# Kernel optimization log

Measured on AMD Instinct MI355X. Metric: run time of the kernel, lower is better.

The kernel has to match this reference:

```python
import jax, jax.numpy as jnp
import numpy as np

E = 100000   # num entities
D = 300      # embedding dim
R = 1000     # num relations
T = 10000    # aligned pairs
K = 25       # negatives per pair
GAMMA = 1.0


def spmm(rows, cols, vals, x, n_rows):
    # sparse(COO) @ dense: out[r] = sum_{nnz: rows==r} vals * x[cols]
    return jax.ops.segment_sum(vals[:, None] * x[cols], rows, num_segments=n_rows)


def setup_inputs() -> dict:
    key = jax.random.key(0)
    ks = jax.random.split(key, 24)
    g = lambda i, s: jax.random.normal(ks[i], s, dtype=jnp.float32) * 0.05
    ri = lambda i, s, hi: jax.random.randint(ks[i], s, 0, hi, dtype=jnp.int32)
    ru = lambda i, s: jax.random.uniform(ks[i], s, dtype=jnp.float32)
    return {
        'word_embedding': jax.random.normal(ks[0], (E, D), dtype=jnp.float32),
        'kernel_gate': g(1, (D, D)),
        'bias_gate': jnp.zeros((D,), jnp.float32),
        'W1': g(2, (D, D)),
        'W2': g(3, (D, D)),
        'Dense': g(4, (3 * D, D)),
        'Bias': jnp.zeros((D,), jnp.float32),
        'hr_rows': ri(5, (300000,), R), 'hr_cols': ri(6, (300000,), E), 'hr_vals': ru(7, (300000,)),
        'tr_rows': ri(8, (300000,), R), 'tr_cols': ri(9, (300000,), E), 'tr_vals': ru(10, (300000,)),
        'er_rows': ri(11, (300000,), E), 'er_cols': ri(12, (300000,), 2 * R), 'er_vals': ru(13, (300000,)),
        'adj_rows': ri(14, (600000,), E), 'adj_cols': ri(15, (600000,), E), 'adj_vals': ru(16, (600000,)),
        'pos_left': ri(17, (T,), E), 'pos_right': ri(18, (T,), E),
        'neg_right': ri(19, (T, K), E), 'neg_left': ri(20, (T, K), E),
        'mask': jnp.ones((T, K), jnp.float32),
    }


def highway(layer1, layer2, kernel_gate, bias_gate):
    tg = jax.nn.sigmoid(layer1 @ kernel_gate + bias_gate)
    return tg * layer2 + (1.0 - tg) * layer1


def reference(word_embedding, kernel_gate, bias_gate, W1, W2, Dense, Bias,
              hr_rows, hr_cols, hr_vals, tr_rows, tr_cols, tr_vals,
              er_rows, er_cols, er_vals, adj_rows, adj_cols, adj_vals,
              pos_left, pos_right, neg_right, neg_left, mask):
    # L2-normalized frozen word embeddings
    emb = word_embedding / jnp.linalg.norm(word_embedding, axis=-1, keepdims=True)

    # Global relation aggregation (compute_r)
    L = spmm(hr_rows, hr_cols, hr_vals, emb, R)          # [R, D]
    Rm = spmm(tr_rows, tr_cols, tr_vals, emb, R)         # [R, D]
    r_fwd = jnp.concatenate([L, Rm], axis=-1)            # [R, 2D]
    r_emb = jnp.concatenate([r_fwd, -r_fwd], axis=0)     # [2R, 2D]
    nb = spmm(er_rows, er_cols, er_vals, r_emb, E)       # [E, 2D]
    h = jnp.concatenate([emb, nb], axis=-1)              # [E, 3D]
    h = emb + jax.nn.relu(h @ Dense + Bias)

    # Local relation aggregation: 2-layer highway GCN
    gcn1 = jax.nn.relu(spmm(adj_rows, adj_cols, adj_vals, h @ W1, E))
    hg1 = highway(h, gcn1, kernel_gate, bias_gate)
    gcn2 = jax.nn.relu(spmm(adj_rows, adj_cols, adj_vals, hg1 @ W2, E))
    node = highway(hg1, gcn2, kernel_gate, bias_gate)    # [E, D]

    # Hinge alignment loss
    l_x = node[pos_left]                                 # [T, D]
    r_x = node[pos_right]                                # [T, D]
    Dm = jnp.sum(jnp.abs(l_x - r_x), axis=1) + GAMMA     # [T]
    B1 = jnp.sum(jnp.abs(l_x[:, None, :] - node[neg_right]), axis=-1)  # [T, K]
    L1 = jax.nn.relu(Dm[:, None] - B1) * mask
    B2 = jnp.sum(jnp.abs(node[neg_left] - r_x[:, None, :]), axis=-1)   # [T, K]
    L2 = jax.nn.relu(Dm[:, None] - B2) * mask
    return (jnp.sum(L1) + jnp.sum(L2)) / 2.0
```

## Files before the change

kernel.cpp:

```cpp
#include <hip/hip_runtime.h>
#include <math.h>

#define E_N 100000
#define D_N 300
#define R_N 1000
#define T_N 10000
#define K_N 25
#define DP  320
#define BM  64
#define NT  1563

#define NB_E   782
#define NB_R   125
#define CAP_AD 256
#define CAP_ER 128
#define CAP_RT 512

typedef __attribute__((ext_vector_type(8))) short bf16x8;
typedef __attribute__((ext_vector_type(4))) float f32x4;

__device__ __forceinline__ float bf2f(unsigned short h){
  union{ unsigned int u; float f; } c; c.u = ((unsigned int)h)<<16; return c.f;
}
__device__ __forceinline__ unsigned short f2bf(float f){
  union{ float f; unsigned int u; } c; c.f = f;
  unsigned int u = c.u + 0x7FFFu + ((c.u>>16)&1u);
  return (unsigned short)(u>>16);
}
__device__ __forceinline__ unsigned int pack2(float lo, float hi){
  return ((unsigned int)f2bf(hi)<<16) | f2bf(lo);
}

static constexpr size_t BUFB   = (size_t)100032*DP*2;
static constexpr size_t BUFU8  = (size_t)100032*DP;
static constexpr size_t OFF_B0    = 0;
static constexpr size_t OFF_B1    = BUFB;
static constexpr size_t OFF_B2    = 2*BUFB;
static constexpr size_t OFF_B3    = 3*BUFB;
static constexpr size_t OFF_RFWD  = OFF_B3 + BUFU8;
static constexpr size_t OFF_G     = OFF_RFWD + 1310720;
static constexpr size_t OFF_WTKG  = OFF_RFWD + 2400000;
static constexpr size_t OFF_WTW1  = OFF_WTKG + 204800;
static constexpr size_t OFF_WTW2  = OFF_WTW1 + 204800;
static constexpr size_t OFF_WTDN  = OFF_WTW2 + 204800;
static constexpr size_t OFF_WTDN2 = OFF_WTDN + 204800;
static constexpr size_t OFF_BIASP = OFF_WTDN2 + 409600;
static constexpr size_t OFF_BGP   = OFF_BIASP + 1280;
static constexpr size_t OFF_PTRHR = OFF_BGP + 1280;
static constexpr size_t OFF_PTRTR = OFF_PTRHR + 4096;
static constexpr size_t OFF_PTRER = OFF_PTRTR + 4096;
static constexpr size_t OFF_PTRADJ= OFF_PTRER + 400896;
static constexpr size_t OFF_CURHR = OFF_PTRADJ + 400896;
static constexpr size_t OFF_CURTR = OFF_CURHR + 4096;
static constexpr size_t OFF_CURER = OFF_CURTR + 4096;
static constexpr size_t OFF_CURADJ= OFF_CURER + 400896;
static constexpr size_t SZ_CURALL = 4096+4096+400896+400896;
static constexpr size_t OFF_SPHR  = OFF_CURADJ + 400896;
static constexpr size_t OFF_SPTR  = OFF_SPHR + 2400000;
static constexpr size_t OFF_SPER  = OFF_SPTR + 2400000;
static constexpr size_t OFF_SPAD  = OFF_SPER + 2400000;
static constexpr size_t OFF_PART  = OFF_SPAD + 4800000;
static constexpr size_t OFF_BSUM  = OFF_PART + 40000;
static constexpr size_t OFF_BCAD  = OFF_BSUM + 4096;
static constexpr size_t OFF_BCER  = OFF_BCAD + 25600;
static constexpr size_t OFF_BCHR  = OFF_BCER + 25600;
static constexpr size_t OFF_BCTR  = OFF_BCHR + 4096;
static constexpr size_t SZ_BCALL  = 25600+25600+4096+4096;
static constexpr size_t OFF_STAD  = OFF_B2;
static constexpr size_t OFF_STER  = OFF_STAD + (size_t)NB_E*8*CAP_AD*8;
static constexpr size_t OFF_STHR  = OFF_STER + (size_t)NB_E*8*CAP_ER*8;
static constexpr size_t OFF_STTR  = OFF_STHR + (size_t)NB_R*8*CAP_RT*8;

__device__ __forceinline__ size_t packIdx(int n, int k, int TK){
  return (size_t)(((n>>4)*TK + (k>>5))<<9) + (((k>>3)&3)<<7) + ((n&15)<<3) + (k&7);
}

__global__ void k_prep_sq(const float* kg, const float* w1, const float* w2,
                          unsigned short* wtKG, unsigned short* wtW1, unsigned short* wtW2){
  int n = blockIdx.x, which = blockIdx.y, k = threadIdx.x;
  const float* src = which==0 ? kg : (which==1 ? w1 : w2);
  unsigned short* dst = which==0 ? wtKG : (which==1 ? wtW1 : wtW2);
  float v = (n < D_N && k < D_N) ? src[k*D_N + n] : 0.f;
  dst[packIdx(n, k, 10)] = f2bf(v);
}

__global__ void k_prep_dense(const float* dn, unsigned short* wt, unsigned short* wt2){
  int n = blockIdx.x, t = threadIdx.x;
  {
    int k = t;
    float v = (n < D_N && k < D_N) ? dn[(size_t)k*D_N + n] : 0.f;
    wt[packIdx(n, k, 10)] = f2bf(v);
  }
  for(int k=t; k<640; k+=320){
    float v = (n < D_N && k < 600) ? dn[(size_t)(300+k)*D_N + n] : 0.f;
    wt2[packIdx(n, k, 20)] = f2bf(v);
  }
}

__global__ void k_prep_bias(const float* bias, const float* bg, float* biasP, float* bgP){
  int t = threadIdx.x;
  biasP[t] = (t < D_N) ? bias[t] : 0.f;
  bgP[t]   = (t < D_N) ? bg[t]   : 0.f;
}

__global__ __launch_bounds__(256) void k_normalize(const float* __restrict__ w,
                                                   unsigned short* __restrict__ embb){
  int wv = threadIdx.x >> 6, lane = threadIdx.x & 63;
  int e = blockIdx.x*4 + wv;
  const float4* row = (const float4*)(w + (size_t)e*D_N);
  float4 x0 = row[lane];
  float4 x1 = make_float4(0.f,0.f,0.f,0.f);
  if(lane < 11) x1 = row[64 + lane];
  float s = x0.x*x0.x + x0.y*x0.y + x0.z*x0.z + x0.w*x0.w
          + x1.x*x1.x + x1.y*x1.y + x1.z*x1.z + x1.w*x1.w;
  #pragma unroll
  for(int off=32; off; off>>=1) s += __shfl_xor(s, off);
  float rn = rsqrtf(s);
  unsigned short* orow = embb + (size_t)e*DP;
  uint2 o0; o0.x = pack2(x0.x*rn, x0.y*rn); o0.y = pack2(x0.z*rn, x0.w*rn);
  *(uint2*)(orow + lane*4) = o0;
  if(lane < 16){
    uint2 o1 = make_uint2(0u,0u);
    if(lane < 11){ o1.x = pack2(x1.x*rn, x1.y*rn); o1.y = pack2(x1.z*rn, x1.w*rn); }
    *(uint2*)(orow + 256 + lane*4) = o1;
  }
}

__global__ __launch_bounds__(256) void k_phaseA(
    const int* hr_r, const int* hr_c, const float* hr_v,
    const int* tr_r, const int* tr_c, const float* tr_v,
    const int* er_r, const int* er_c, const float* er_v,
    const int* ad_r, const int* ad_c, const float* ad_v,
    int* cHR, int* cTR, int* cER, int* cAD,
    int* bcHR, int* bcTR, int* bcER, int* bcAD,
    uint2* stHR, uint2* stTR, uint2* stER, uint2* stAD){
  int g8 = blockIdx.x & 7;
  int i = (blockIdx.x*256 + threadIdx.x)*2;
  const int* rp; const int* cp; const float* vp; int* cnt; int* bc; uint2* st;
  int j, shift, cap;
  if(i < 300000){ rp=hr_r; cp=hr_c; vp=hr_v; cnt=cHR; bc=bcHR; st=stHR; j=i;        shift=3; cap=CAP_RT; }
  else if(i < 600000){ rp=tr_r; cp=tr_c; vp=tr_v; cnt=cTR; bc=bcTR; st=stTR; j=i-300000; shift=3; cap=CAP_RT; }
  else if(i < 900000){ rp=er_r; cp=er_c; vp=er_v; cnt=cER; bc=bcER; st=stER; j=i-600000; shift=7; cap=CAP_ER; }
  else if(i < 1500000){ rp=ad_r; cp=ad_c; vp=ad_v; cnt=cAD; bc=bcAD; st=stAD; j=i-900000; shift=7; cap=CAP_AD; }
  else return;
  int2 r = *(const int2*)(rp + j);
  int2 c = *(const int2*)(cp + j);
  float2 v = *(const float2*)(vp + j);
  atomicAdd(&cnt[r.x], 1);
  atomicAdd(&cnt[r.y], 1);
  int m = (1<<shift) - 1;
  int sb0 = ((r.x>>shift)<<3) + g8;
  int sb1 = ((r.y>>shift)<<3) + g8;
  int p0 = atomicAdd(&bc[sb0], 1);
  int p1 = atomicAdd(&bc[sb1], 1);
  st[(size_t)sb0*cap + p0] = make_uint2(((unsigned)(r.x&m)<<17)|(unsigned)c.x, __float_as_uint(v.x));
  st[(size_t)sb1*cap + p1] = make_uint2(((unsigned)(r.y&m)<<17)|(unsigned)c.y, __float_as_uint(v.y));
}

__global__ __launch_bounds__(256) void k_bscatter(
    const uint2* __restrict__ stAD, const uint2* __restrict__ stER,
    const uint2* __restrict__ stHR, const uint2* __restrict__ stTR,
    const int* __restrict__ bcAD, const int* __restrict__ bcER,
    const int* __restrict__ bcHR, const int* __restrict__ bcTR,
    const int* __restrict__ pAD, const int* __restrict__ pER,
    const int* __restrict__ pHR, const int* __restrict__ pTR,
    uint2* spAD, uint2* spER, uint2* spHR, uint2* spTR){
  __shared__ int cur[128];
  int b = blockIdx.x, tid = threadIdx.x;
  const uint2* st; const int* bc; const int* ptr; uint2* sp;
  int base, nrows, cap, maxrow;
  if(b < NB_E){            st=stAD; bc=bcAD; ptr=pAD; sp=spAD; base=b;           nrows=128; cap=CAP_AD; maxrow=E_N; }
  else if(b < 2*NB_E){     st=stER; bc=bcER; ptr=pER; sp=spER; base=b-NB_E;      nrows=128; cap=CAP_ER; maxrow=E_N; }
  else if(b < 2*NB_E+NB_R){st=stHR; bc=bcHR; ptr=pHR; sp=spHR; base=b-2*NB_E;    nrows=8;   cap=CAP_RT; maxrow=R_N; }
  else {                   st=stTR; bc=bcTR; ptr=pTR; sp=spTR; base=b-2*NB_E-NB_R; nrows=8; cap=CAP_RT; maxrow=R_N; }
  int r0 = base*nrows;
  if(tid < nrows){
    int row = r0 + tid;
    cur[tid] = (row < maxrow) ? ptr[row] : 0;
  }
  __syncthreads();
  #pragma unroll 1
  for(int s=0; s<8; s++){
    int sb = base*8 + s;
    int cnt = bc[sb];
    const uint2* src = st + (size_t)sb*cap;
    for(int j=tid; j<cnt; j+=256){
      uint2 q = src[j];
      int rl = (int)(q.x >> 17);
      unsigned col = q.x & 0x1FFFFu;
      int p = atomicAdd(&cur[rl], 1);
      sp[p] = make_uint2(col, q.y);
    }
  }
}

__global__ void k_scan_small(int* cHR, int* cTR, int* pHR, int* pTR){
  __shared__ int s[1024];
  int t = threadIdx.x;
  for(int w=0; w<2; w++){
    int* cnt = w ? cTR : cHR; int* ptr = w ? pTR : pHR;
    int c = (t < R_N) ? cnt[t] : 0;
    s[t] = c; __syncthreads();
    for(int off=1; off<1024; off<<=1){
      int v = (t>=off) ? s[t-off] : 0; __syncthreads();
      s[t] += v; __syncthreads();
    }
    if(t < R_N) ptr[t] = s[t] - c;
    if(t == R_N-1) ptr[R_N] = s[t];
    __syncthreads();
  }
}

__global__ void k_scan_part(const int* cER, const int* cAD, int* pER, int* pAD, int* bsum){
  int which = blockIdx.y;
  const int* cnt = which ? cAD : cER;
  int* ptr = which ? pAD : pER;
  __shared__ int s[1024];
  int g = blockIdx.x, t = threadIdx.x, i = g*1024 + t;
  int c = (i < E_N) ? cnt[i] : 0;
  s[t] = c; __syncthreads();
  for(int off=1; off<1024; off<<=1){
    int v = (t>=off) ? s[t-off] : 0; __syncthreads();
    s[t] += v; __syncthreads();
  }
  if(i < E_N) ptr[i] = s[t] - c;
  if(t == 1023) bsum[which*128 + g] = s[1023];
}

__global__ void k_scan_mid(int* bsum, int* pER, int* pAD){
  __shared__ int s[128];
  int t = threadIdx.x;
  for(int w=0; w<2; w++){
    int v = (t < 98) ? bsum[w*128 + t] : 0;
    s[t] = v; __syncthreads();
    for(int off=1; off<128; off<<=1){
      int u = (t>=off) ? s[t-off] : 0; __syncthreads();
      s[t] += u; __syncthreads();
    }
    if(t < 98) bsum[w*128 + t] = s[t] - v;
    if(t == 97){ int* p = w ? pAD : pER; p[E_N] = s[97]; }
    __syncthreads();
  }
}

__global__ void k_scan_add(const int* bsum, int* pER, int* pAD){
  int which = blockIdx.y;
  int* ptr = which ? pAD : pER;
  int g = blockIdx.x, i = g*1024 + threadIdx.x;
  if(i < E_N) ptr[i] += bsum[which*128 + g];
}

__global__ __launch_bounds__(256) void k_spmm_rel(
    const int* __restrict__ ptr, const uint2* __restrict__ sp,
    const unsigned short* __restrict__ embb, unsigned short* __restrict__ rfwdb, int off){
  int w = threadIdx.x >> 6, lane = threadIdx.x & 63;
  int r = blockIdx.x*2 + (w>>1);
  int half = w & 1;
  int elem = half*160 + 4*lane;
  bool act = (lane < 40) && (elem < 300);
  int b = ptr[r], e2 = ptr[r+1];
  float a0=0.f, a1=0.f, a2=0.f, a3=0.f;
  if(act){
    const unsigned short* base = embb + elem;
    int j = b;
    for(; j+4 <= e2; j += 4){
      uint2 q0=sp[j], q1=sp[j+1], q2=sp[j+2], q3=sp[j+3];
      int c0=(int)q0.x, c1=(int)q1.x, c2=(int)q2.x, c3=(int)q3.x;
      float v0=__uint_as_float(q0.y), v1=__uint_as_float(q1.y),
            v2=__uint_as_float(q2.y), v3=__uint_as_float(q3.y);
      uint2 x0 = *(const uint2*)(base + (size_t)c0*DP);
      uint2 x1 = *(const uint2*)(base + (size_t)c1*DP);
      uint2 x2 = *(const uint2*)(base + (size_t)c2*DP);
      uint2 x3 = *(const uint2*)(base + (size_t)c3*DP);
      a0 += v0*bf2f(x0.x&0xFFFF) + v1*bf2f(x1.x&0xFFFF) + v2*bf2f(x2.x&0xFFFF) + v3*bf2f(x3.x&0xFFFF);
      a1 += v0*bf2f(x0.x>>16)    + v1*bf2f(x1.x>>16)    + v2*bf2f(x2.x>>16)    + v3*bf2f(x3.x>>16);
      a2 += v0*bf2f(x0.y&0xFFFF) + v1*bf2f(x1.y&0xFFFF) + v2*bf2f(x2.y&0xFFFF) + v3*bf2f(x3.y&0xFFFF);
      a3 += v0*bf2f(x0.y>>16)    + v1*bf2f(x1.y>>16)    + v2*bf2f(x2.y>>16)    + v3*bf2f(x3.y>>16);
    }
    for(; j < e2; j++){
      uint2 q = sp[j];
      int c = (int)q.x; float v = __uint_as_float(q.y);
      uint2 x = *(const uint2*)(base + (size_t)c*DP);
      a0 += v*bf2f(x.x&0xFFFF); a1 += v*bf2f(x.x>>16);
      a2 += v*bf2f(x.y&0xFFFF); a3 += v*bf2f(x.y>>16);
    }
    uint2 o;
    o.x = pack2(a0, a1);
    o.y = pack2(a2, a3);
    *(uint2*)&rfwdb[(size_t)r*640 + off + elem] = o;
  }
}

__global__ __launch_bounds__(256) void k_gemm_G(const unsigned short* __restrict__ rfwdb,
    const unsigned short* __restrict__ Bt2, unsigned short* __restrict__ G){
  __shared__ unsigned short bufG[64][640];
  int tid = threadIdx.x;
  int wave = tid>>6, lane = tid&63, quad = lane>>4, l16 = lane&15;
  int m0 = blockIdx.x * 64;
  #pragma unroll
  for(int i=0; i<20; i++){
    int idx = tid + i*256;
    int row = idx/80, colc = idx%80;
    *(uint4*)&bufG[row][(colc ^ (row&7))*8] = *(const uint4*)(rfwdb + (size_t)(m0+row)*640 + colc*8);
  }
  __syncthreads();
  f32x4 acc[4][5];
  #pragma unroll
  for(int mf=0; mf<4; mf++)
    #pragma unroll
    for(int nf=0; nf<5; nf++) acc[mf][nf] = (f32x4){0.f,0.f,0.f,0.f};
  #pragma unroll 2
  for(int kk=0; kk<640; kk+=32){
    bf16x8 af[4], bfr[5];
    #pragma unroll
    for(int mf=0; mf<4; mf++)
      af[mf] = *(const bf16x8*)&bufG[mf*16 + l16][(((kk>>3)+quad) ^ (l16&7))*8];
    #pragma unroll
    for(int nf=0; nf<5; nf++)
      bfr[nf] = *(const bf16x8*)(Bt2 + ((size_t)(((wave*5+nf)*20 + (kk>>5))<<6) + lane)*8);
    #pragma unroll
    for(int mf=0; mf<4; mf++)
      #pragma unroll
      for(int nf=0; nf<5; nf++)
        acc[mf][nf] = __builtin_amdgcn_mfma_f32_16x16x32_bf16(af[mf], bfr[nf], acc[mf][nf], 0, 0, 0);
  }
  __syncthreads();
  unsigned short (*ob)[DP] = (unsigned short(*)[DP])bufG;
  #pragma unroll
  for(int mf=0; mf<4; mf++)
    #pragma unroll
    for(int nf=0; nf<5; nf++){
      int col = wave*80 + nf*16 + l16;
      #pragma unroll
      for(int i=0; i<4; i++){
        int rowl = mf*16 + quad*4 + i;
        ob[rowl][((col>>3) ^ (rowl&7))*8 + (col&7)] = f2bf(acc[mf][nf][i]);
      }
    }
  __syncthreads();
  #pragma unroll
  for(int i=0; i<10; i++){
    int idx = tid + i*256;
    int row = idx/40, colc = idx%40;
    *(uint4*)(G + (size_t)(m0+row)*DP + colc*8) = *(const uint4*)&ob[row][(colc ^ (row&7))*8];
  }
}

__global__ __launch_bounds__(256) void k_er_g(
    const int* __restrict__ ptr, const uint2* __restrict__ sp,
    const unsigned short* __restrict__ G, unsigned short* __restrict__ nb){
  int w = threadIdx.x >> 6, lane = threadIdx.x & 63;
  int e = blockIdx.x*4 + w;
  int b = ptr[e], en = ptr[e+1];
  if(lane < 40){
    float a0[8], a1[8];
    #pragma unroll
    for(int i=0;i<8;i++){ a0[i]=0.f; a1[i]=0.f; }
    const unsigned short* gb = G + lane*8;
    int j = b;
    for(; j+2 <= en; j += 2){
      uint2 q0=sp[j], q1=sp[j+1];
      int c0=(int)q0.x, c1=(int)q1.x;
      float v0=__uint_as_float(q0.y), v1=__uint_as_float(q1.y);
      int p0=c0, p1=c1;
      if(c0 >= R_N){ p0 = c0-R_N; v0 = -v0; }
      if(c1 >= R_N){ p1 = c1-R_N; v1 = -v1; }
      bf16x8 x0 = *(const bf16x8*)(gb + (size_t)p0*DP);
      bf16x8 x1 = *(const bf16x8*)(gb + (size_t)p1*DP);
      #pragma unroll
      for(int i=0;i<8;i++){ a0[i] += v0*bf2f((unsigned short)x0[i]);
                            a1[i] += v1*bf2f((unsigned short)x1[i]); }
    }
    if(j < en){
      uint2 q = sp[j];
      int c=(int)q.x; float v=__uint_as_float(q.y);
      int p=c; if(c >= R_N){ p = c-R_N; v = -v; }
      bf16x8 x = *(const bf16x8*)(gb + (size_t)p*DP);
      #pragma unroll
      for(int i=0;i<8;i++) a0[i] += v*bf2f((unsigned short)x[i]);
    }
    bf16x8 o;
    #pragma unroll
    for(int i=0;i<8;i++) o[i] = (short)f2bf(a0[i]+a1[i]);
    *(bf16x8*)&nb[(size_t)e*DP + lane*8] = o;
  }
}

__global__ __launch_bounds__(256) void k_spmm_hw(
    const int* __restrict__ ptr, const uint2* __restrict__ sp,
    const unsigned short* __restrict__ hw, const unsigned char* __restrict__ tg,
    const unsigned short* __restrict__ res, unsigned short* __restrict__ out){
  int w = threadIdx.x >> 6, lane = threadIdx.x & 63;
  int e = blockIdx.x*4 + w;
  int b = ptr[e], en = ptr[e+1];
  if(lane < 40){
    float a0[8], a1[8];
    #pragma unroll
    for(int i=0;i<8;i++){ a0[i]=0.f; a1[i]=0.f; }
    const unsigned short* base = hw + lane*8;
    int j = b;
    for(; j+2 <= en; j += 2){
      uint2 q0=sp[j], q1=sp[j+1];
      int c0=(int)q0.x, c1=(int)q1.x;
      float v0=__uint_as_float(q0.y), v1=__uint_as_float(q1.y);
      bf16x8 x0 = *(const bf16x8*)(base + (size_t)c0*DP);
      bf16x8 x1 = *(const bf16x8*)(base + (size_t)c1*DP);
      #pragma unroll
      for(int i=0;i<8;i++){ a0[i] += v0 * bf2f((unsigned short)x0[i]);
                            a1[i] += v1 * bf2f((unsigned short)x1[i]); }
    }
    if(j < en){
      uint2 q = sp[j];
      int c = (int)q.x; float v = __uint_as_float(q.y);
      bf16x8 x = *(const bf16x8*)(base + (size_t)c*DP);
      #pragma unroll
      for(int i=0;i<8;i++) a0[i] += v * bf2f((unsigned short)x[i]);
    }
    uint2 tu = *(const uint2*)(tg + (size_t)e*DP + lane*8);
    bf16x8 rv = *(const bf16x8*)(res + (size_t)e*DP + lane*8);
    bf16x8 o;
    #pragma unroll
    for(int i=0;i<8;i++){
      unsigned int word = (i<4) ? tu.x : tu.y;
      float g = (float)((word >> ((i&3)*8)) & 255u);
      g = (g + 0.5f) * 0.00390625f;
      float gcn = fmaxf(a0[i]+a1[i], 0.f);
      o[i] = (short)f2bf(g*gcn + (1.f-g)*bf2f(rv[i]));
    }
    *(bf16x8*)&out[(size_t)e*DP + lane*8] = o;
  }
}

__device__ __forceinline__ void stageA(unsigned short (*buf)[DP],
                                       const unsigned short* __restrict__ src, int tid){
  #pragma unroll
  for(int i=0; i<10; i++){
    int idx = tid + i*256;
    int row = idx/40, colc = idx%40;
    *(uint4*)&buf[row][(colc ^ (row&7))*8] = *(const uint4*)(src + (size_t)idx*8);
  }
}
__device__ __forceinline__ void storeT(unsigned short* dst,
                                       const unsigned short (*buf)[DP], int tid){
  #pragma unroll
  for(int i=0; i<10; i++){
    int idx = tid + i*256;
    int row = idx/40, colc = idx%40;
    *(uint4*)(dst + (size_t)idx*8) = *(const uint4*)&buf[row][(colc ^ (row&7))*8];
  }
}
__device__ __forceinline__ void storeT16(unsigned short* __restrict__ dst,
                                         const unsigned short (*buf)[DP], int tid){
  #pragma unroll
  for(int i=0; i<3; i++){
    int idx = tid + i*256;
    if(idx < 640){
      int row = idx/40, colc = idx%40;
      *(uint4*)(dst + (size_t)idx*8) = *(const uint4*)&buf[row][(colc ^ (row&7))*8];
    }
  }
}
__device__ __forceinline__ void kloop(f32x4 acc[4][5], const unsigned short (*As)[DP],
    const unsigned short* __restrict__ Bt, int TK, int tkb, int wave, int quad, int l16){
  int lane = (quad<<4) | l16;
  #pragma unroll 2
  for(int kk=0; kk<DP; kk+=32){
    bf16x8 af[4], bfr[5];
    #pragma unroll
    for(int mf=0; mf<4; mf++)
      af[mf] = *(const bf16x8*)&As[mf*16 + l16][(((kk>>3)+quad) ^ (l16&7))*8];
    #pragma unroll
    for(int nf=0; nf<5; nf++)
      bfr[nf] = *(const bf16x8*)(Bt + ((size_t)(((wave*5+nf)*TK + tkb + (kk>>5))<<6) + lane)*8);
    #pragma unroll
    for(int mf=0; mf<4; mf++)
      #pragma unroll
      for(int nf=0; nf<5; nf++)
        acc[mf][nf] = __builtin_amdgcn_mfma_f32_16x16x32_bf16(af[mf], bfr[nf], acc[mf][nf], 0, 0, 0);
  }
}

__global__ __launch_bounds__(256,3) void k_gemm_f(
    const unsigned short* __restrict__ Ain,
    const unsigned short* __restrict__ BtD,
    const unsigned short* nbG,
    const float* __restrict__ biasP,
    const unsigned short* __restrict__ BtW,
    const unsigned short* __restrict__ BtG,
    const float* __restrict__ bgP,
    unsigned short* hOut,
    unsigned short* __restrict__ hwOut,
    unsigned char*  __restrict__ tgOut,
    int dense){
  __shared__ unsigned short buf[BM][DP];
  __shared__ unsigned short scr[16][DP];
  int tid = threadIdx.x;
  int wave = tid>>6, lane = tid&63, quad = lane>>4, l16 = lane&15;
  int m0 = blockIdx.x * BM;

  stageA(buf, Ain + (size_t)m0*DP, tid);
  __syncthreads();

  if(dense){
    float breg[5];
    #pragma unroll
    for(int nf=0; nf<5; nf++) breg[nf] = biasP[wave*80 + nf*16 + l16];
    f32x4 acc[4][5];
    #pragma unroll
    for(int mf=0; mf<4; mf++)
      #pragma unroll
      for(int nf=0; nf<5; nf++) acc[mf][nf] = (f32x4){0.f,0.f,0.f,0.f};
    kloop(acc, buf, BtD, 10, 0, wave, quad, l16);
    const unsigned short* nbrow = nbG + (size_t)m0*DP;
    #pragma unroll
    for(int mf=0; mf<4; mf++){
      #pragma unroll
      for(int i=0; i<3; i++){
        int idx = tid + i*256;
        if(idx < 640){
          int row = idx/40, colc = idx%40;
          *(uint4*)&scr[row][(colc ^ (row&7))*8] =
              *(const uint4*)(nbrow + (size_t)(mf*16+row)*DP + colc*8);
        }
      }
      __syncthreads();
      #pragma unroll
      for(int nf=0; nf<5; nf++){
        int col = wave*80 + nf*16 + l16;
        #pragma unroll
        for(int i=0; i<4; i++){
          int rowl = mf*16 + quad*4 + i;
          int rloc = quad*4 + i;
          int a = ((col>>3) ^ (rowl&7))*8 + (col&7);
          float nbv  = bf2f(scr[rloc][((col>>3) ^ (rloc&7))*8 + (col&7)]);
          float resv = bf2f(buf[rowl][a]);
          buf[rowl][a] = f2bf(resv + fmaxf(acc[mf][nf][i] + breg[nf] + nbv, 0.f));
        }
      }
      __syncthreads();
    }
    storeT(hOut + (size_t)m0*DP, buf, tid);
  }

  {
    f32x4 acc[4][5];
    #pragma unroll
    for(int mf=0; mf<4; mf++)
      #pragma unroll
      for(int nf=0; nf<5; nf++) acc[mf][nf] = (f32x4){0.f,0.f,0.f,0.f};
    kloop(acc, buf, BtW, 10, 0, wave, quad, l16);
    #pragma unroll
    for(int mf=0; mf<4; mf++){
      #pragma unroll
      for(int nf=0; nf<5; nf++){
        int col = wave*80 + nf*16 + l16;
        #pragma unroll
        for(int i=0; i<4; i++){
          int rowl = quad*4 + i;
          scr[rowl][((col>>3) ^ (rowl&7))*8 + (col&7)] = f2bf(acc[mf][nf][i]);
        }
      }
      __syncthreads();
      storeT16(hwOut + (size_t)(m0 + mf*16)*DP, scr, tid);
      __syncthreads();
    }
  }

  {
    float greg[5];
    #pragma unroll
    for(int nf=0; nf<5; nf++) greg[nf] = bgP[wave*80 + nf*16 + l16];
    f32x4 acc[4][5];
    #pragma unroll
    for(int mf=0; mf<4; mf++)
      #pragma unroll
      for(int nf=0; nf<5; nf++) acc[mf][nf] = (f32x4){0.f,0.f,0.f,0.f};
    kloop(acc, buf, BtG, 10, 0, wave, quad, l16);
    unsigned char* bu = (unsigned char*)scr;
    #pragma unroll
    for(int c=0; c<2; c++){
      #pragma unroll
      for(int mh=0; mh<2; mh++){
        int mf = c*2 + mh;
        #pragma unroll
        for(int nf=0; nf<5; nf++){
          int col = wave*80 + nf*16 + l16;
          #pragma unroll
          for(int i=0; i<4; i++){
            int rowl = mh*16 + quad*4 + i;
            float tg = 1.f / (1.f + expf(-(acc[mf][nf][i] + greg[nf])));
            int u = (int)(tg * 256.f);
            u = u < 0 ? 0 : (u > 255 ? 255 : u);
            bu[rowl*DP + col] = (unsigned char)u;
          }
        }
      }
      __syncthreads();
      unsigned char* dst = tgOut + (size_t)(m0 + c*32)*DP;
      #pragma unroll
      for(int i=0; i<3; i++){
        int idx = tid + i*256;
        if(idx < 640) *(uint4*)(dst + (size_t)idx*16) = *(const uint4*)(bu + (size_t)idx*16);
      }
      __syncthreads();
    }
  }
}

__global__ __launch_bounds__(256) void k_loss(const unsigned short* __restrict__ node,
                       const int* __restrict__ pl, const int* __restrict__ pr,
                       const int* __restrict__ nr, const int* __restrict__ nl,
                       const float* __restrict__ mask,
                       float* __restrict__ part){
  int t = blockIdx.x;
  int w = threadIdx.x >> 6, lane = threadIdx.x & 63;
  __shared__ float wsum[4];
  bool act = lane < 40;
  size_t lb = (size_t)pl[t]*DP, rb = (size_t)pr[t]*DP;
  float lv[8], rv[8];
  #pragma unroll
  for(int i=0;i<8;i++){ lv[i]=0.f; rv[i]=0.f; }
  if(act){
    bf16x8 L = *(const bf16x8*)&node[lb + lane*8];
    bf16x8 R = *(const bf16x8*)&node[rb + lane*8];
    #pragma unroll
    for(int i=0;i<8;i++){ lv[i]=bf2f((unsigned short)L[i]); rv[i]=bf2f((unsigned short)R[i]); }
  }
  float s = 0.f;
  #pragma unroll
  for(int i=0;i<8;i++) s += fabsf(lv[i] - rv[i]);
  #pragma unroll
  for(int off=32; off; off>>=1) s += __shfl_xor(s, off);
  float dm = s + 1.0f;

  float local = 0.f;
  for(int k=w; k<K_N; k+=8){
    int k2 = k + 4;
    bool h2 = k2 < K_N;
    int kb = h2 ? k2 : k;
    float s1a=0.f, s2a=0.f, s1b=0.f, s2b=0.f;
    if(act){
      size_t nrb  = (size_t)nr[t*K_N+k ]*DP, nlb  = (size_t)nl[t*K_N+k ]*DP;
      size_t nrb2 = (size_t)nr[t*K_N+kb]*DP, nlb2 = (size_t)nl[t*K_N+kb]*DP;
      bf16x8 X1 = *(const bf16x8*)&node[nrb  + lane*8];
      bf16x8 Y1 = *(const bf16x8*)&node[nlb  + lane*8];
      bf16x8 X2 = *(const bf16x8*)&node[nrb2 + lane*8];
      bf16x8 Y2 = *(const bf16x8*)&node[nlb2 + lane*8];
      #pragma unroll
      for(int i=0;i<8;i++){
        s1a += fabsf(lv[i] - bf2f((unsigned short)X1[i]));
        s2a += fabsf(bf2f((unsigned short)Y1[i]) - rv[i]);
        s1b += fabsf(lv[i] - bf2f((unsigned short)X2[i]));
        s2b += fabsf(bf2f((unsigned short)Y2[i]) - rv[i]);
      }
    }
    #pragma unroll
    for(int off=32; off; off>>=1){
      s1a += __shfl_xor(s1a, off); s2a += __shfl_xor(s2a, off);
      s1b += __shfl_xor(s1b, off); s2b += __shfl_xor(s2b, off);
    }
    if(lane==0){
      local += (fmaxf(dm - s1a, 0.f) + fmaxf(dm - s2a, 0.f)) * mask[t*K_N+k];
      if(h2) local += (fmaxf(dm - s1b, 0.f) + fmaxf(dm - s2b, 0.f)) * mask[t*K_N+k2];
    }
  }
  if(lane==0) wsum[w] = local;
  __syncthreads();
  if(threadIdx.x==0) part[t] = wsum[0]+wsum[1]+wsum[2]+wsum[3];
}

__global__ void k_reduce(const float* part, float* out){
  __shared__ float s[256];
  int t = threadIdx.x;
  float a = 0.f;
  for(int i=t; i<T_N; i+=256) a += part[i];
  s[t] = a; __syncthreads();
  for(int off=128; off; off>>=1){ if(t<off) s[t]+=s[t+off]; __syncthreads(); }
  if(t==0) out[0] = s[0]*0.5f;
}

extern "C" void kernel_launch(void* const* d_in, const int* in_sizes, int n_in,
                              void* d_out, int out_size, void* d_ws, size_t ws_size,
                              hipStream_t stream){
  const float* Wemb = (const float*)d_in[0];
  const float* KG   = (const float*)d_in[1];
  const float* BG   = (const float*)d_in[2];
  const float* W1   = (const float*)d_in[3];
  const float* W2   = (const float*)d_in[4];
  const float* DN   = (const float*)d_in[5];
  const float* BI   = (const float*)d_in[6];
  const int* HRr = (const int*)d_in[7];  const int* HRc = (const int*)d_in[8];  const float* HRv = (const float*)d_in[9];
  const int* TRr = (const int*)d_in[10]; const int* TRc = (const int*)d_in[11]; const float* TRv = (const float*)d_in[12];
  const int* ERr = (const int*)d_in[13]; const int* ERc = (const int*)d_in[14]; const float* ERv = (const float*)d_in[15];
  const int* ADr = (const int*)d_in[16]; const int* ADc = (const int*)d_in[17]; const float* ADv = (const float*)d_in[18];
  const int* PL = (const int*)d_in[19]; const int* PR = (const int*)d_in[20];
  const int* NR = (const int*)d_in[21]; const int* NL = (const int*)d_in[22];
  const float* MASK = (const float*)d_in[23];
  char* ws = (char*)d_ws;

  unsigned short* B0 = (unsigned short*)(ws + OFF_B0);
  unsigned short* B1 = (unsigned short*)(ws + OFF_B1);
  unsigned short* B2 = (unsigned short*)(ws + OFF_B2);
  unsigned char*  B3 = (unsigned char*)(ws + OFF_B3);
  unsigned short* rfwdb = (unsigned short*)(ws + OFF_RFWD);
  unsigned short* Gb    = (unsigned short*)(ws + OFF_G);
  unsigned short* wtKG = (unsigned short*)(ws + OFF_WTKG);
  unsigned short* wtW1 = (unsigned short*)(ws + OFF_WTW1);
  unsigned short* wtW2 = (unsigned short*)(ws + OFF_WTW2);
  unsigned short* wtDN = (unsigned short*)(ws + OFF_WTDN);
  unsigned short* wtDN2= (unsigned short*)(ws + OFF_WTDN2);
  float* biasP = (float*)(ws + OFF_BIASP);
  float* bgP   = (float*)(ws + OFF_BGP);
  int* pHR = (int*)(ws + OFF_PTRHR); int* pTR = (int*)(ws + OFF_PTRTR);
  int* pER = (int*)(ws + OFF_PTRER); int* pAD = (int*)(ws + OFF_PTRADJ);
  int* cHR = (int*)(ws + OFF_CURHR); int* cTR = (int*)(ws + OFF_CURTR);
  int* cER = (int*)(ws + OFF_CURER); int* cAD = (int*)(ws + OFF_CURADJ);
  uint2* spHR = (uint2*)(ws + OFF_SPHR);
  uint2* spTR = (uint2*)(ws + OFF_SPTR);
  uint2* spER = (uint2*)(ws + OFF_SPER);
  uint2* spAD = (uint2*)(ws + OFF_SPAD);
  float* part = (float*)(ws + OFF_PART);
  int* bsum   = (int*)(ws + OFF_BSUM);
  int* bcAD = (int*)(ws + OFF_BCAD); int* bcER = (int*)(ws + OFF_BCER);
  int* bcHR = (int*)(ws + OFF_BCHR); int* bcTR = (int*)(ws + OFF_BCTR);
  uint2* stAD = (uint2*)(ws + OFF_STAD); uint2* stER = (uint2*)(ws + OFF_STER);
  uint2* stHR = (uint2*)(ws + OFF_STHR); uint2* stTR = (uint2*)(ws + OFF_STTR);

  (void)hipMemsetAsync(ws + OFF_CURHR, 0, SZ_CURALL, stream);
  (void)hipMemsetAsync(ws + OFF_BCAD, 0, SZ_BCALL, stream);
  (void)hipMemsetAsync(ws + OFF_RFWD, 0, 1310720, stream);

  k_prep_sq<<<dim3(320,3), 320, 0, stream>>>(KG, W1, W2, wtKG, wtW1, wtW2);
  k_prep_dense<<<320, 320, 0, stream>>>(DN, wtDN, wtDN2);
  k_prep_bias<<<1, 320, 0, stream>>>(BI, BG, biasP, bgP);
  k_normalize<<<E_N/4, 256, 0, stream>>>(Wemb, B0);

  k_phaseA<<<2930, 256, 0, stream>>>(HRr,HRc,HRv, TRr,TRc,TRv, ERr,ERc,ERv, ADr,ADc,ADv,
                                     cHR,cTR,cER,cAD, bcHR,bcTR,bcER,bcAD,
                                     stHR,stTR,stER,stAD);
  k_scan_small<<<1, 1024, 0, stream>>>(cHR, cTR, pHR, pTR);
  k_scan_part<<<dim3(98,2), 1024, 0, stream>>>(cER, cAD, pER, pAD, bsum);
  k_scan_mid<<<1, 128, 0, stream>>>(bsum, pER, pAD);
  k_scan_add<<<dim3(98,2), 1024, 0, stream>>>(bsum, pER, pAD);
  k_bscatter<<<2*NB_E + 2*NB_R, 256, 0, stream>>>(stAD, stER, stHR, stTR,
                                                  bcAD, bcER, bcHR, bcTR,
                                                  pAD, pER, pHR, pTR,
                                                  spAD, spER, spHR, spTR);

  k_spmm_rel<<<R_N/2, 256, 0, stream>>>(pHR, spHR, B0, rfwdb, 0);
  k_spmm_rel<<<R_N/2, 256, 0, stream>>>(pTR, spTR, B0, rfwdb, 300);

  k_gemm_G<<<16, 256, 0, stream>>>(rfwdb, wtDN2, Gb);
  k_er_g<<<E_N/4, 256, 0, stream>>>(pER, spER, Gb, B1);

  k_gemm_f<<<NT, 256, 0, stream>>>(B0, wtDN, B1, biasP,
                                   wtW1, wtKG, bgP, B1, B2, B3, 1);
  k_spmm_hw<<<E_N/4, 256, 0, stream>>>(pAD, spAD, B2, B3, B1, B0);
  k_gemm_f<<<NT, 256, 0, stream>>>(B0, nullptr, nullptr, nullptr,
                                   wtW2, wtKG, bgP, nullptr, B2, B3, 0);
  k_spmm_hw<<<E_N/4, 256, 0, stream>>>(pAD, spAD, B2, B3, B0, B1);

  k_loss<<<T_N, 256, 0, stream>>>(B1, PL, PR, NR, NL, MASK, part);
  k_reduce<<<1, 256, 0, stream>>>(part, (float*)d_out);
}
```

Before: 1.095 ms.

## Replace global per-row count atomics with shared-memory histogram over staged buckets

The bucketing pass no longer does a global atomicAdd per nonzero into per-row count arrays. A new k_bcount kernel rebuilds each row's count from the staged buckets using a shared-memory histogram per block. The staging layout also changes from bucket-major to group-major (g8*nbst + bucket), so the 8 group counters for a bucket are spread apart rather than adjacent. This removes 1.5M scattered global atomics and one memset, at the cost of an extra kernel launch and a second read of the staged data.

```diff
diff --git a/kernel.cpp b/kernel.cpp
--- a/kernel.cpp
+++ b/kernel.cpp
@@ -15,6 +15,8 @@
 #define CAP_AD 256
 #define CAP_ER 128
 #define CAP_RT 512
+#define BCS_E  1024
+#define BCS_R  128
 
 typedef __attribute__((ext_vector_type(8))) short bf16x8;
 typedef __attribute__((ext_vector_type(4))) float f32x4;
@@ -50,26 +52,25 @@
 static constexpr size_t OFF_PTRTR = OFF_PTRHR + 4096;
 static constexpr size_t OFF_PTRER = OFF_PTRTR + 4096;
 static constexpr size_t OFF_PTRADJ= OFF_PTRER + 400896;
-static constexpr size_t OFF_CURHR = OFF_PTRADJ + 400896;
-static constexpr size_t OFF_CURTR = OFF_CURHR + 4096;
-static constexpr size_t OFF_CURER = OFF_CURTR + 4096;
-static constexpr size_t OFF_CURADJ= OFF_CURER + 400896;
-static constexpr size_t SZ_CURALL = 4096+4096+400896+400896;
-static constexpr size_t OFF_SPHR  = OFF_CURADJ + 400896;
+static constexpr size_t OFF_CHR   = OFF_PTRADJ + 400896;
+static constexpr size_t OFF_CTR   = OFF_CHR + 4096;
+static constexpr size_t OFF_CER   = OFF_CTR + 4096;
+static constexpr size_t OFF_CAD   = OFF_CER + 400896;
+static constexpr size_t OFF_SPHR  = OFF_CAD + 400896;
 static constexpr size_t OFF_SPTR  = OFF_SPHR + 2400000;
 static constexpr size_t OFF_SPER  = OFF_SPTR + 2400000;
 static constexpr size_t OFF_SPAD  = OFF_SPER + 2400000;
 static constexpr size_t OFF_PART  = OFF_SPAD + 4800000;
 static constexpr size_t OFF_BSUM  = OFF_PART + 40000;
 static constexpr size_t OFF_BCAD  = OFF_BSUM + 4096;
-static constexpr size_t OFF_BCER  = OFF_BCAD + 25600;
-static constexpr size_t OFF_BCHR  = OFF_BCER + 25600;
+static constexpr size_t OFF_BCER  = OFF_BCAD + 32768;
+static constexpr size_t OFF_BCHR  = OFF_BCER + 32768;
 static constexpr size_t OFF_BCTR  = OFF_BCHR + 4096;
-static constexpr size_t SZ_BCALL  = 25600+25600+4096+4096;
+static constexpr size_t SZ_BCALL  = 32768+32768+4096+4096;
 static constexpr size_t OFF_STAD  = OFF_B2;
-static constexpr size_t OFF_STER  = OFF_STAD + (size_t)NB_E*8*CAP_AD*8;
-static constexpr size_t OFF_STHR  = OFF_STER + (size_t)NB_E*8*CAP_ER*8;
-static constexpr size_t OFF_STTR  = OFF_STHR + (size_t)NB_R*8*CAP_RT*8;
+static constexpr size_t OFF_STER  = OFF_STAD + (size_t)8*NB_E*CAP_AD*8;
+static constexpr size_t OFF_STHR  = OFF_STER + (size_t)8*NB_E*CAP_ER*8;
+static constexpr size_t OFF_STTR  = OFF_STHR + (size_t)8*NB_R*CAP_RT*8;
 
 __device__ __forceinline__ size_t packIdx(int n, int k, int TK){
   return (size_t)(((n>>4)*TK + (k>>5))<<9) + (((k>>3)&3)<<7) + ((n&15)<<3) + (k&7);
@@ -131,30 +132,54 @@
     const int* tr_r, const int* tr_c, const float* tr_v,
     const int* er_r, const int* er_c, const float* er_v,
     const int* ad_r, const int* ad_c, const float* ad_v,
-    int* cHR, int* cTR, int* cER, int* cAD,
     int* bcHR, int* bcTR, int* bcER, int* bcAD,
     uint2* stHR, uint2* stTR, uint2* stER, uint2* stAD){
   int g8 = blockIdx.x & 7;
   int i = (blockIdx.x*256 + threadIdx.x)*2;
-  const int* rp; const int* cp; const float* vp; int* cnt; int* bc; uint2* st;
-  int j, shift, cap;
-  if(i < 300000){ rp=hr_r; cp=hr_c; vp=hr_v; cnt=cHR; bc=bcHR; st=stHR; j=i;        shift=3; cap=CAP_RT; }
-  else if(i < 600000){ rp=tr_r; cp=tr_c; vp=tr_v; cnt=cTR; bc=bcTR; st=stTR; j=i-300000; shift=3; cap=CAP_RT; }
-  else if(i < 900000){ rp=er_r; cp=er_c; vp=er_v; cnt=cER; bc=bcER; st=stER; j=i-600000; shift=7; cap=CAP_ER; }
-  else if(i < 1500000){ rp=ad_r; cp=ad_c; vp=ad_v; cnt=cAD; bc=bcAD; st=stAD; j=i-900000; shift=7; cap=CAP_AD; }
+  const int* rp; const int* cp; const float* vp; int* bc; uint2* st;
+  int j, shift, cap, nbst, bcs;
+  if(i < 300000){      rp=hr_r; cp=hr_c; vp=hr_v; bc=bcHR; st=stHR; j=i;        shift=3; cap=CAP_RT; nbst=NB_R; bcs=BCS_R; }
+  else if(i < 600000){ rp=tr_r; cp=tr_c; vp=tr_v; bc=bcTR; st=stTR; j=i-300000; shift=3; cap=CAP_RT; nbst=NB_R; bcs=BCS_R; }
+  else if(i < 900000){ rp=er_r; cp=er_c; vp=er_v; bc=bcER; st=stER; j=i-600000; shift=7; cap=CAP_ER; nbst=NB_E; bcs=BCS_E; }
+  else if(i < 1500000){rp=ad_r; cp=ad_c; vp=ad_v; bc=bcAD; st=stAD; j=i-900000; shift=7; cap=CAP_AD; nbst=NB_E; bcs=BCS_E; }
   else return;
   int2 r = *(const int2*)(rp + j);
   int2 c = *(const int2*)(cp + j);
   float2 v = *(const float2*)(vp + j);
-  atomicAdd(&cnt[r.x], 1);
-  atomicAdd(&cnt[r.y], 1);
   int m = (1<<shift) - 1;
-  int sb0 = ((r.x>>shift)<<3) + g8;
-  int sb1 = ((r.y>>shift)<<3) + g8;
-  int p0 = atomicAdd(&bc[sb0], 1);
-  int p1 = atomicAdd(&bc[sb1], 1);
-  st[(size_t)sb0*cap + p0] = make_uint2(((unsigned)(r.x&m)<<17)|(unsigned)c.x, __float_as_uint(v.x));
-  st[(size_t)sb1*cap + p1] = make_uint2(((unsigned)(r.y&m)<<17)|(unsigned)c.y, __float_as_uint(v.y));
+  int b0 = r.x>>shift, b1 = r.y>>shift;
+  int p0 = atomicAdd(&bc[g8*bcs + b0], 1);
+  int p1 = atomicAdd(&bc[g8*bcs + b1], 1);
+  st[(size_t)(g8*nbst + b0)*cap + p0] = make_uint2(((unsigned)(r.x&m)<<17)|(unsigned)c.x, __float_as_uint(v.x));
+  st[(size_t)(g8*nbst + b1)*cap + p1] = make_uint2(((unsigned)(r.y&m)<<17)|(unsigned)c.y, __float_as_uint(v.y));
+}
+
+__global__ __launch_bounds__(256) void k_bcount(
+    const uint2* __restrict__ stAD, const uint2* __restrict__ stER,
+    const uint2* __restrict__ stHR, const uint2* __restrict__ stTR,
+    const int* __restrict__ bcAD, const int* __restrict__ bcER,
+    const int* __restrict__ bcHR, const int* __restrict__ bcTR,
+    int* cAD, int* cER, int* cHR, int* cTR){
+  __shared__ int hist[128];
+  int b = blockIdx.x, tid = threadIdx.x;
+  const uint2* st; const int* bc; int* cnt;
+  int base, nrows, cap, maxrow, nbst, bcs;
+  if(b < NB_E){            st=stAD; bc=bcAD; cnt=cAD; base=b;             nrows=128; cap=CAP_AD; maxrow=E_N; nbst=NB_E; bcs=BCS_E; }
+  else if(b < 2*NB_E){     st=stER; bc=bcER; cnt=cER; base=b-NB_E;        nrows=128; cap=CAP_ER; maxrow=E_N; nbst=NB_E; bcs=BCS_E; }
+  else if(b < 2*NB_E+NB_R){st=stHR; bc=bcHR; cnt=cHR; base=b-2*NB_E;      nrows=8;   cap=CAP_RT; maxrow=R_N; nbst=NB_R; bcs=BCS_R; }
+  else {                   st=stTR; bc=bcTR; cnt=cTR; base=b-2*NB_E-NB_R; nrows=8;   cap=CAP_RT; maxrow=R_N; nbst=NB_R; bcs=BCS_R; }
+  if(tid < nrows) hist[tid] = 0;
+  __syncthreads();
+  #pragma unroll 1
+  for(int s=0; s<8; s++){
+    int n = bc[s*bcs + base];
+    const uint2* src = st + (size_t)(s*nbst + base)*cap;
+    for(int j=tid; j<n; j+=256)
+      atomicAdd(&hist[src[j].x >> 17], 1);
+  }
+  __syncthreads();
+  int row = base*nrows + tid;
+  if(tid < nrows && row < maxrow) cnt[row] = hist[tid];
 }
 
 __global__ __launch_bounds__(256) void k_bscatter(
@@ -168,11 +193,11 @@
   __shared__ int cur[128];
   int b = blockIdx.x, tid = threadIdx.x;
   const uint2* st; const int* bc; const int* ptr; uint2* sp;
-  int base, nrows, cap, maxrow;
-  if(b < NB_E){            st=stAD; bc=bcAD; ptr=pAD; sp=spAD; base=b;           nrows=128; cap=CAP_AD; maxrow=E_N; }
-  else if(b < 2*NB_E){     st=stER; bc=bcER; ptr=pER; sp=spER; base=b-NB_E;      nrows=128; cap=CAP_ER; maxrow=E_N; }
-  else if(b < 2*NB_E+NB_R){st=stHR; bc=bcHR; ptr=pHR; sp=spHR; base=b-2*NB_E;    nrows=8;   cap=CAP_RT; maxrow=R_N; }
-  else {                   st=stTR; bc=bcTR; ptr=pTR; sp=spTR; base=b-2*NB_E-NB_R; nrows=8; cap=CAP_RT; maxrow=R_N; }
+  int base, nrows, cap, maxrow, nbst, bcs;
+  if(b < NB_E){            st=stAD; bc=bcAD; ptr=pAD; sp=spAD; base=b;             nrows=128; cap=CAP_AD; maxrow=E_N; nbst=NB_E; bcs=BCS_E; }
+  else if(b < 2*NB_E){     st=stER; bc=bcER; ptr=pER; sp=spER; base=b-NB_E;        nrows=128; cap=CAP_ER; maxrow=E_N; nbst=NB_E; bcs=BCS_E; }
+  else if(b < 2*NB_E+NB_R){st=stHR; bc=bcHR; ptr=pHR; sp=spHR; base=b-2*NB_E;      nrows=8;   cap=CAP_RT; maxrow=R_N; nbst=NB_R; bcs=BCS_R; }
+  else {                   st=stTR; bc=bcTR; ptr=pTR; sp=spTR; base=b-2*NB_E-NB_R; nrows=8;   cap=CAP_RT; maxrow=R_N; nbst=NB_R; bcs=BCS_R; }
   int r0 = base*nrows;
   if(tid < nrows){
     int row = r0 + tid;
@@ -181,10 +206,9 @@
   __syncthreads();
   #pragma unroll 1
   for(int s=0; s<8; s++){
-    int sb = base*8 + s;
-    int cnt = bc[sb];
-    const uint2* src = st + (size_t)sb*cap;
-    for(int j=tid; j<cnt; j+=256){
+    int n = bc[s*bcs + base];
+    const uint2* src = st + (size_t)(s*nbst + base)*cap;
+    for(int j=tid; j<n; j+=256){
       uint2 q = src[j];
       int rl = (int)(q.x >> 17);
       unsigned col = q.x & 0x1FFFFu;
@@ -713,8 +737,8 @@
   float* bgP   = (float*)(ws + OFF_BGP);
   int* pHR = (int*)(ws + OFF_PTRHR); int* pTR = (int*)(ws + OFF_PTRTR);
   int* pER = (int*)(ws + OFF_PTRER); int* pAD = (int*)(ws + OFF_PTRADJ);
-  int* cHR = (int*)(ws + OFF_CURHR); int* cTR = (int*)(ws + OFF_CURTR);
-  int* cER = (int*)(ws + OFF_CURER); int* cAD = (int*)(ws + OFF_CURADJ);
+  int* cHR = (int*)(ws + OFF_CHR); int* cTR = (int*)(ws + OFF_CTR);
+  int* cER = (int*)(ws + OFF_CER); int* cAD = (int*)(ws + OFF_CAD);
   uint2* spHR = (uint2*)(ws + OFF_SPHR);
   uint2* spTR = (uint2*)(ws + OFF_SPTR);
   uint2* spER = (uint2*)(ws + OFF_SPER);
@@ -726,7 +750,6 @@
   uint2* stAD = (uint2*)(ws + OFF_STAD); uint2* stER = (uint2*)(ws + OFF_STER);
   uint2* stHR = (uint2*)(ws + OFF_STHR); uint2* stTR = (uint2*)(ws + OFF_STTR);
 
-  (void)hipMemsetAsync(ws + OFF_CURHR, 0, SZ_CURALL, stream);
   (void)hipMemsetAsync(ws + OFF_BCAD, 0, SZ_BCALL, stream);
   (void)hipMemsetAsync(ws + OFF_RFWD, 0, 1310720, stream);
 
@@ -736,8 +759,10 @@
   k_normalize<<<E_N/4, 256, 0, stream>>>(Wemb, B0);
 
   k_phaseA<<<2930, 256, 0, stream>>>(HRr,HRc,HRv, TRr,TRc,TRv, ERr,ERc,ERv, ADr,ADc,ADv,
-                                     cHR,cTR,cER,cAD, bcHR,bcTR,bcER,bcAD,
-                                     stHR,stTR,stER,stAD);
+                                     bcHR,bcTR,bcER,bcAD, stHR,stTR,stER,stAD);
+  k_bcount<<<2*NB_E + 2*NB_R, 256, 0, stream>>>(stAD, stER, stHR, stTR,
+                                                bcAD, bcER, bcHR, bcTR,
+                                                cAD, cER, cHR, cTR);
   k_scan_small<<<1, 1024, 0, stream>>>(cHR, cTR, pHR, pTR);
   k_scan_part<<<dim3(98,2), 1024, 0, stream>>>(cER, cAD, pER, pAD, bsum);
   k_scan_mid<<<1, 128, 0, stream>>>(bsum, pER, pAD);
```

Measured after the change: 983.7 us. 1.11x faster.
